# Optimization experiments

Measured on AMD Instinct MI355X. Metric: run time of the kernel, lower is better.

Reference implementation:

```python
import jax, jax.numpy as jnp
import numpy as np

# Static configuration (matches init_kwargs)
L = 3264          # seq_length
K = 12            # ktc=4 -> K=12
LOCC = 4          # ktc=4 -> Locc=4
S, B, A = 8, 64, 4  # streams (user/port pairs), batch, rx antennas
DELAY_MIN, DELAY_MAX = -10, 10


def _phasor(m):
    # m: integer shifts [S, B] -> exp(1j*2*pi*m*n/L) as [S, B, L]
    n = jnp.arange(L, dtype=jnp.int32)
    ang = (2.0 * np.pi / L) * ((m[..., None] * n) % L).astype(jnp.float32)
    return jax.lax.complex(jnp.cos(ang), jnp.sin(ang))


def _linear_interp(h_avg):
    # np.interp with uniform source grid orig[i] = (LOCC-1)/2 + i*LOCC, clamped at ends.
    # h_avg: [S, B, A, R] complex, R = L // LOCC -> [S, B, A, L]
    R = L // LOCC
    new = jnp.arange(L, dtype=jnp.float32)
    t = jnp.clip((new - (LOCC - 1) / 2.0) / LOCC, 0.0, float(R - 1))
    i0 = jnp.floor(t).astype(jnp.int32)
    i1 = jnp.minimum(i0 + 1, R - 1)
    frac = (t - i0).astype(jnp.float32)
    return h_avg[..., i0] * (1.0 - frac) + h_avg[..., i1] * frac


def reference(ls_real, ls_imag, cyclic_shifts, noise_powers):
    ls = jax.lax.complex(ls_real, ls_imag)                     # [S,B,A,L]
    ideal_peak = ((K - cyclic_shifts) % K) * (L // K)          # [S]

    # Stage 1: IFFT + timing-offset search (torch.no_grad in original)
    h_time = jnp.fft.ifft(ls, axis=-1)
    power = jax.lax.stop_gradient(jnp.sum(jnp.abs(h_time) ** 2, axis=2))  # [S,B,L]
    offs = jnp.arange(DELAY_MIN, DELAY_MAX + 1, dtype=jnp.int32)          # [21]
    cand_idx = (ideal_peak[:, None] + offs[None, :]) % L                   # [S,21]
    cand_idx = jnp.broadcast_to(cand_idx[:, None, :], (S, B, offs.shape[0]))
    cand_pow = jnp.take_along_axis(power, cand_idx, axis=-1)               # [S,B,21]
    t_off = offs[jnp.argmax(cand_pow, axis=-1)]                            # [S,B]
    m = t_off + ideal_peak[:, None]                                        # [S,B]
    ph_m = _phasor(m)        # [S,B,L]
    ph_T = _phasor(t_off)    # [S,B,L]

    # Stage 2: phasor shift, OCC demux, interpolation (inside no_grad in original)
    h_shift = ls * ph_m[:, :, None, :]
    h_avg = h_shift.reshape(S, B, A, L // LOCC, LOCC).mean(-1)             # [S,B,A,L/4]
    h_interp = jax.lax.stop_gradient(_linear_interp(h_avg))                # [S,B,A,L]

    # Stage 3: global residual against stream (0,0)'s LS estimate
    total_recon = jnp.sum(h_interp * jnp.conj(ph_m)[:, :, None, :], axis=0)  # [B,A,L]
    residual = ls[0] - total_recon                                           # [B,A,L]

    # Stage 4: apply residual, MMSE (identity: mmse_module=None), timing recovery
    h_wr = h_interp + residual[None, :, :, None, :].squeeze(3) if False else h_interp + residual[None] * ph_m[:, :, None, :]
    final = h_wr * jnp.conj(ph_T)[:, :, None, :]                             # [S,B,A,L]
    return jnp.stack([final.real, final.imag]).astype(jnp.float32)          # [2,S,B,A,L]


def setup_inputs() -> dict:
    key = jax.random.key(0)
    k1, k2, k3, k4 = jax.random.split(key, 4)
    return {
        "ls_real": jax.random.normal(k1, (S, B, A, L), dtype=jnp.float32),
        "ls_imag": jax.random.normal(k2, (S, B, A, L), dtype=jnp.float32),
        "cyclic_shifts": jax.random.randint(k3, (S,), 0, K, dtype=jnp.int32),
        "noise_powers": jax.random.uniform(k4, (B,), dtype=jnp.float32),
    }
```

## Files before the change

kernel.cpp:

```cpp
#include <hip/hip_runtime.h>

namespace {

constexpr int L = 3264;
constexpr int K = 12;
constexpr int S = 8;
constexpr int B = 64;
constexpr int A = 4;
constexpr int R = 816;
constexpr int NOFF = 21;
constexpr int PEAK_STEP = L / K;
constexpr float TWO_PI = 6.28318530717958647692f;
constexpr float CINV = TWO_PI / (float)L;
constexpr int NCHUNK = (L + 255) / 256;

__device__ __forceinline__ float rfl(float x) {
    return __uint_as_float(__builtin_amdgcn_readfirstlane(__float_as_uint(x)));
}

__global__ __launch_bounds__(256)
void k_table(float2* __restrict__ tw)
{
    const int j = blockIdx.x * 256 + threadIdx.x;
    if (j < L) {
        float sv, cv;
        __sincosf(CINV * (float)j, &sv, &cv);
        tw[j] = make_float2(cv, sv);
    }
}

__global__ __launch_bounds__(512)
void k_stage1(const float* __restrict__ lsr, const float* __restrict__ lsi,
              const int* __restrict__ cs, const float2* __restrict__ tw,
              int* __restrict__ toff_out, int* __restrict__ m_out,
              float2* __restrict__ havg)
{
    __shared__ float2 red[8][NOFF];
    __shared__ int m_sh;

    const int sb = blockIdx.x;
    const int s = sb >> 6;
    const int tid = threadIdx.x;
    const int lane = tid & 63;
    const int w = tid >> 6;
    const int a = w >> 1;
    const int h = w & 1;

    const int csv = cs[s];
    const int ideal = ((K - csv) % K) * PEAK_STEP;
    int idx0 = (ideal - 10) % L; if (idx0 < 0) idx0 += L;

    const int k0 = h * 64 + lane;

    const int jb = (k0 * idx0) % L;
    float br, bi; __sincosf(CINV * (float)jb, &bi, &br);
    float lr, li; __sincosf(CINV * (float)k0, &li, &lr);
    float pwr[NOFF], pwi[NOFF];
    pwr[0] = br; pwi[0] = bi;
    #pragma unroll
    for (int d = 1; d < NOFF; ++d) {
        pwr[d] = pwr[d-1] * lr - pwi[d-1] * li;
        pwi[d] = pwr[d-1] * li + pwi[d-1] * lr;
    }

    const int js = (128 * idx0) % L;
    float s0r, s0i; __sincosf(CINV * (float)js, &s0i, &s0r);
    float e8r, e8i; __sincosf(CINV * 128.0f, &e8i, &e8r);
    float str_[NOFF], sti_[NOFF];
    {
        float cr = s0r, ci = s0i;
        #pragma unroll
        for (int d = 0; d < NOFF; ++d) {
            str_[d] = rfl(cr); sti_[d] = rfl(ci);
            const float nr = cr * e8r - ci * e8i;
            ci = cr * e8i + ci * e8r;
            cr = nr;
        }
    }

    const size_t rowbase = ((size_t)sb * A + a) * L;
    const float* __restrict__ pr = lsr + rowbase;
    const float* __restrict__ pi_ = lsi + rowbase;

    float ar[NOFF], ai[NOFF];
    #pragma unroll
    for (int d = 0; d < NOFF; ++d) { ar[d] = 0.f; ai[d] = 0.f; }

    for (int it = 0; it < 25; ++it) {
        const float xr = pr[k0 + (it << 7)];
        const float xi = pi_[k0 + (it << 7)];
        #pragma unroll
        for (int d = 0; d < NOFF; ++d) {
            ar[d] += xr * pwr[d] - xi * pwi[d];
            ai[d] += xr * pwi[d] + xi * pwr[d];
            const float nr = pwr[d] * str_[d] - pwi[d] * sti_[d];
            pwi[d] = pwr[d] * sti_[d] + pwi[d] * str_[d];
            pwr[d] = nr;
        }
    }
    if (k0 < 64) {
        const float xr = pr[k0 + 3200];
        const float xi = pi_[k0 + 3200];
        #pragma unroll
        for (int d = 0; d < NOFF; ++d) {
            ar[d] += xr * pwr[d] - xi * pwi[d];
            ai[d] += xr * pwi[d] + xi * pwr[d];
        }
    }

    #pragma unroll
    for (int d = 0; d < NOFF; ++d) {
        float r = ar[d], im = ai[d];
        #pragma unroll
        for (int o = 32; o > 0; o >>= 1) {
            r  += __shfl_xor(r, o);
            im += __shfl_xor(im, o);
        }
        if (lane == 0) red[w][d] = make_float2(r, im);
    }
    __syncthreads();

    if (w == 0) {
        float pw = -1.f;
        if (lane < NOFF) {
            pw = 0.f;
            #pragma unroll
            for (int a2 = 0; a2 < A; ++a2) {
                const float2 u = red[2 * a2][lane];
                const float2 v = red[2 * a2 + 1][lane];
                const float rr = u.x + v.x;
                const float ii = u.y + v.y;
                pw += rr * rr + ii * ii;
            }
        }
        float mx = pw;
        #pragma unroll
        for (int o = 32; o > 0; o >>= 1) mx = fmaxf(mx, __shfl_xor(mx, o));
        const unsigned long long msk = __ballot(pw == mx);
        const int argd = __ffsll(msk) - 1;
        if (lane == 0) {
            const int toff = argd - 10;
            toff_out[sb] = toff;
            m_out[sb]    = toff + ideal;
            m_sh         = toff + ideal;
        }
    }
    __syncthreads();

    int mp = m_sh % L; if (mp < 0) mp += L;
    const float2 emp = tw[mp];

    for (int aa = 0; aa < A; ++aa) {
        const float4* __restrict__ qr4 = (const float4*)(lsr + ((size_t)sb * A + aa) * L);
        const float4* __restrict__ qi4 = (const float4*)(lsi + ((size_t)sb * A + aa) * L);
        float2* __restrict__ dst = havg + ((size_t)sb * A + aa) * R;
        for (int i = tid; i < R; i += 512) {
            const int j = (mp * (4 * i)) % L;
            const float2 w0 = tw[j];
            const float4 xr = qr4[i];
            const float4 xi = qi4[i];
            float wr = w0.x, wi = w0.y;
            float are, aim, nr;
            are  = xr.x * wr - xi.x * wi;  aim  = xr.x * wi + xi.x * wr;
            nr = wr * emp.x - wi * emp.y;  wi = wr * emp.y + wi * emp.x;  wr = nr;
            are += xr.y * wr - xi.y * wi;  aim += xr.y * wi + xi.y * wr;
            nr = wr * emp.x - wi * emp.y;  wi = wr * emp.y + wi * emp.x;  wr = nr;
            are += xr.z * wr - xi.z * wi;  aim += xr.z * wi + xi.z * wr;
            nr = wr * emp.x - wi * emp.y;  wi = wr * emp.y + wi * emp.x;  wr = nr;
            are += xr.w * wr - xi.w * wi;  aim += xr.w * wi + xi.w * wr;
            dst[i] = make_float2(are * 0.25f, aim * 0.25f);
        }
    }
}

__global__ __launch_bounds__(256)
void k_final(const float* __restrict__ lsr, const float* __restrict__ lsi,
             const int* __restrict__ toff_arr, const int* __restrict__ m_arr,
             const float2* __restrict__ havg, const float2* __restrict__ tw,
             float* __restrict__ out)
{
    const int bid = blockIdx.x;
    const int chunk = bid % NCHUNK;
    const int ba = bid / NCHUNK;
    const int b = ba >> 2;
    const int a = ba & 3;
    const int l = chunk * 256 + (int)threadIdx.x;
    if (l >= L) return;

    float t = ((float)l - 1.5f) * 0.25f;
    t = fminf(fmaxf(t, 0.0f), (float)(R - 1));
    const int i0 = (int)t;
    const int i1 = min(i0 + 1, R - 1);
    const float frac = t - (float)i0;

    float hire[S], hiim[S], pmre[S], pmim[S];
    float rre = 0.f, rim = 0.f;

    #pragma unroll
    for (int s = 0; s < S; ++s) {
        const int sb = s * B + b;
        int mp = m_arr[sb] % L; if (mp < 0) mp += L;
        const float2 wm = tw[(mp * l) % L];
        const float2 h0 = havg[((size_t)sb * A + a) * R + i0];
        const float2 h1 = havg[((size_t)sb * A + a) * R + i1];
        const float hr = h0.x * (1.f - frac) + h1.x * frac;
        const float hi = h0.y * (1.f - frac) + h1.y * frac;
        hire[s] = hr; hiim[s] = hi; pmre[s] = wm.x; pmim[s] = wm.y;
        rre += hr * wm.x + hi * wm.y;
        rim += hi * wm.x - hr * wm.y;
    }

    const size_t off0 = ((size_t)(b * A + a)) * L + l;
    const float resre = lsr[off0] - rre;
    const float resim = lsi[off0] - rim;

    #pragma unroll
    for (int s = 0; s < S; ++s) {
        const float wre = hire[s] + resre * pmre[s] - resim * pmim[s];
        const float wim = hiim[s] + resre * pmim[s] + resim * pmre[s];
        int jt = (toff_arr[s * B + b] * l) % L; if (jt < 0) jt += L;
        const float2 wt = tw[jt];
        const float fre = wre * wt.x + wim * wt.y;
        const float fim = wim * wt.x - wre * wt.y;
        const size_t o = (((size_t)(s * B + b)) * A + a) * L + l;
        __builtin_nontemporal_store(fre, &out[o]);
        __builtin_nontemporal_store(fim, &out[(size_t)S * B * A * L + o]);
    }
}

}

extern "C" void kernel_launch(void* const* d_in, const int* in_sizes, int n_in,
                              void* d_out, int out_size, void* d_ws, size_t ws_size,
                              hipStream_t stream) {
    (void)in_sizes; (void)n_in; (void)out_size; (void)ws_size;
    const float* lsr = (const float*)d_in[0];
    const float* lsi = (const float*)d_in[1];
    const int*   cs  = (const int*)d_in[2];

    int* toff = (int*)d_ws;
    int* marr = toff + 512;
    float2* tw = (float2*)((char*)d_ws + 4096);
    float2* havg = (float2*)((char*)d_ws + 36864);

    k_table<<<NCHUNK, 256, 0, stream>>>(tw);
    k_stage1<<<S * B, 512, 0, stream>>>(lsr, lsi, cs, tw, toff, marr, havg);
    k_final<<<B * A * NCHUNK, 256, 0, stream>>>(lsr, lsi, toff, marr, havg, tw,
                                                (float*)d_out);
}
```

Baseline: 180.8 us.

## Split stage1 into per-antenna DFT, argmax and havg kernels; cache twiddles in LDS

The fused stage1 kernel, one block per stream-batch pair, is split into three kernels. A per-antenna DFT kernel writes candidate powers to a workspace buffer, a small argmax kernel picks the timing offset, and a per-antenna averaging kernel builds havg. This gives four times as many blocks and more parallelism for the DFT and demux work, at the cost of two extra launches and a global round trip for the powers. The final kernel also copies the twiddle table into shared memory so its scattered gathers avoid global loads, at the cost of a per-block preload and sync.

```diff
diff --git a/kernel.cpp b/kernel.cpp
--- a/kernel.cpp
+++ b/kernel.cpp
@@ -29,78 +29,69 @@
     }
 }
 
-__global__ __launch_bounds__(512)
-void k_stage1(const float* __restrict__ lsr, const float* __restrict__ lsi,
-              const int* __restrict__ cs, const float2* __restrict__ tw,
-              int* __restrict__ toff_out, int* __restrict__ m_out,
-              float2* __restrict__ havg)
-{
-    __shared__ float2 red[8][NOFF];
-    __shared__ int m_sh;
-
-    const int sb = blockIdx.x;
+__global__ __launch_bounds__(256)
+void k_dft(const float* __restrict__ lsr, const float* __restrict__ lsi,
+           const int* __restrict__ cs, float* __restrict__ pow_out)
+{
+    __shared__ float2 red[4][NOFF];
+
+    const int blk = blockIdx.x;
+    const int sb = blk >> 2;
+    const int a = blk & 3;
     const int s = sb >> 6;
     const int tid = threadIdx.x;
     const int lane = tid & 63;
     const int w = tid >> 6;
-    const int a = w >> 1;
-    const int h = w & 1;
-
-    const int csv = cs[s];
-    const int ideal = ((K - csv) % K) * PEAK_STEP;
+
+    const int ideal = ((K - cs[s]) % K) * PEAK_STEP;
     int idx0 = (ideal - 10) % L; if (idx0 < 0) idx0 += L;
 
-    const int k0 = h * 64 + lane;
-
-    const int jb = (k0 * idx0) % L;
+    const int jb = (tid * idx0) % L;
     float br, bi; __sincosf(CINV * (float)jb, &bi, &br);
-    float lr, li; __sincosf(CINV * (float)k0, &li, &lr);
-    float pwr[NOFF], pwi[NOFF];
+    float lr, li; __sincosf(CINV * (float)tid, &li, &lr);
+    float pwr[NOFF], pwi[NOFF], ar[NOFF], ai[NOFF];
     pwr[0] = br; pwi[0] = bi;
     #pragma unroll
     for (int d = 1; d < NOFF; ++d) {
         pwr[d] = pwr[d-1] * lr - pwi[d-1] * li;
         pwi[d] = pwr[d-1] * li + pwi[d-1] * lr;
     }
-
-    const int js = (128 * idx0) % L;
+    #pragma unroll
+    for (int d = 0; d < NOFF; ++d) { ar[d] = 0.f; ai[d] = 0.f; }
+
+    const int js = (256 * idx0) % L;
     float s0r, s0i; __sincosf(CINV * (float)js, &s0i, &s0r);
-    float e8r, e8i; __sincosf(CINV * 128.0f, &e8i, &e8r);
+    float c8r, c8i; __sincosf(CINV * 256.0f, &c8i, &c8r);
     float str_[NOFF], sti_[NOFF];
     {
         float cr = s0r, ci = s0i;
         #pragma unroll
         for (int d = 0; d < NOFF; ++d) {
             str_[d] = rfl(cr); sti_[d] = rfl(ci);
-            const float nr = cr * e8r - ci * e8i;
-            ci = cr * e8i + ci * e8r;
-            cr = nr;
-        }
-    }
-
-    const size_t rowbase = ((size_t)sb * A + a) * L;
-    const float* __restrict__ pr = lsr + rowbase;
-    const float* __restrict__ pi_ = lsi + rowbase;
-
-    float ar[NOFF], ai[NOFF];
-    #pragma unroll
-    for (int d = 0; d < NOFF; ++d) { ar[d] = 0.f; ai[d] = 0.f; }
-
-    for (int it = 0; it < 25; ++it) {
-        const float xr = pr[k0 + (it << 7)];
-        const float xi = pi_[k0 + (it << 7)];
+            const float nr2 = cr * c8r - ci * c8i;
+            ci = cr * c8i + ci * c8r;
+            cr = nr2;
+        }
+    }
+
+    const float* __restrict__ pr  = lsr + (size_t)blk * L;
+    const float* __restrict__ pi_ = lsi + (size_t)blk * L;
+
+    for (int it = 0; it < 12; ++it) {
+        const float xr = pr[tid + (it << 8)];
+        const float xi = pi_[tid + (it << 8)];
         #pragma unroll
         for (int d = 0; d < NOFF; ++d) {
             ar[d] += xr * pwr[d] - xi * pwi[d];
             ai[d] += xr * pwi[d] + xi * pwr[d];
-            const float nr = pwr[d] * str_[d] - pwi[d] * sti_[d];
+            const float nr2 = pwr[d] * str_[d] - pwi[d] * sti_[d];
             pwi[d] = pwr[d] * sti_[d] + pwi[d] * str_[d];
-            pwr[d] = nr;
-        }
-    }
-    if (k0 < 64) {
-        const float xr = pr[k0 + 3200];
-        const float xi = pi_[k0 + 3200];
+            pwr[d] = nr2;
+        }
+    }
+    if (tid < 192) {
+        const float xr = pr[tid + 3072];
+        const float xi = pi_[tid + 3072];
         #pragma unroll
         for (int d = 0; d < NOFF; ++d) {
             ar[d] += xr * pwr[d] - xi * pwi[d];
@@ -120,56 +111,71 @@
     }
     __syncthreads();
 
-    if (w == 0) {
-        float pw = -1.f;
-        if (lane < NOFF) {
-            pw = 0.f;
-            #pragma unroll
-            for (int a2 = 0; a2 < A; ++a2) {
-                const float2 u = red[2 * a2][lane];
-                const float2 v = red[2 * a2 + 1][lane];
-                const float rr = u.x + v.x;
-                const float ii = u.y + v.y;
-                pw += rr * rr + ii * ii;
-            }
-        }
-        float mx = pw;
-        #pragma unroll
-        for (int o = 32; o > 0; o >>= 1) mx = fmaxf(mx, __shfl_xor(mx, o));
-        const unsigned long long msk = __ballot(pw == mx);
-        const int argd = __ffsll(msk) - 1;
-        if (lane == 0) {
-            const int toff = argd - 10;
-            toff_out[sb] = toff;
-            m_out[sb]    = toff + ideal;
-            m_sh         = toff + ideal;
-        }
-    }
-    __syncthreads();
-
-    int mp = m_sh % L; if (mp < 0) mp += L;
+    if (w == 0 && lane < NOFF) {
+        float rr = 0.f, ii = 0.f;
+        #pragma unroll
+        for (int q = 0; q < 4; ++q) { rr += red[q][lane].x; ii += red[q][lane].y; }
+        pow_out[sb * (NOFF * A) + lane * A + a] = rr * rr + ii * ii;
+    }
+}
+
+__global__ __launch_bounds__(64)
+void k_argmax(const float* __restrict__ pow_in, const int* __restrict__ cs,
+              int* __restrict__ toff_out, int* __restrict__ m_out)
+{
+    const int sb = blockIdx.x;
+    const int lane = threadIdx.x;
+    const int s = sb >> 6;
+    const int ideal = ((K - cs[s]) % K) * PEAK_STEP;
+
+    float pw = -1.f;
+    if (lane < NOFF) {
+        const float4 p4 = *(const float4*)(pow_in + sb * (NOFF * A) + lane * A);
+        pw = p4.x + p4.y + p4.z + p4.w;
+    }
+    float mx = pw;
+    #pragma unroll
+    for (int o = 32; o > 0; o >>= 1) mx = fmaxf(mx, __shfl_xor(mx, o));
+    const unsigned long long msk = __ballot(pw == mx);
+    const int argd = __ffsll(msk) - 1;
+    if (lane == 0) {
+        const int toff = argd - 10;
+        toff_out[sb] = toff;
+        m_out[sb]    = toff + ideal;
+    }
+}
+
+__global__ __launch_bounds__(256)
+void k_havg(const float* __restrict__ lsr, const float* __restrict__ lsi,
+            const int* __restrict__ m_arr, const float2* __restrict__ tw,
+            float2* __restrict__ havg)
+{
+    const int blk = blockIdx.x;
+    const int sb = blk >> 2;
+    const int tid = threadIdx.x;
+
+    int mp = m_arr[sb] % L; if (mp < 0) mp += L;
     const float2 emp = tw[mp];
 
-    for (int aa = 0; aa < A; ++aa) {
-        const float4* __restrict__ qr4 = (const float4*)(lsr + ((size_t)sb * A + aa) * L);
-        const float4* __restrict__ qi4 = (const float4*)(lsi + ((size_t)sb * A + aa) * L);
-        float2* __restrict__ dst = havg + ((size_t)sb * A + aa) * R;
-        for (int i = tid; i < R; i += 512) {
-            const int j = (mp * (4 * i)) % L;
-            const float2 w0 = tw[j];
-            const float4 xr = qr4[i];
-            const float4 xi = qi4[i];
-            float wr = w0.x, wi = w0.y;
-            float are, aim, nr;
-            are  = xr.x * wr - xi.x * wi;  aim  = xr.x * wi + xi.x * wr;
-            nr = wr * emp.x - wi * emp.y;  wi = wr * emp.y + wi * emp.x;  wr = nr;
-            are += xr.y * wr - xi.y * wi;  aim += xr.y * wi + xi.y * wr;
-            nr = wr * emp.x - wi * emp.y;  wi = wr * emp.y + wi * emp.x;  wr = nr;
-            are += xr.z * wr - xi.z * wi;  aim += xr.z * wi + xi.z * wr;
-            nr = wr * emp.x - wi * emp.y;  wi = wr * emp.y + wi * emp.x;  wr = nr;
-            are += xr.w * wr - xi.w * wi;  aim += xr.w * wi + xi.w * wr;
-            dst[i] = make_float2(are * 0.25f, aim * 0.25f);
-        }
+    const float4* __restrict__ qr4 = (const float4*)(lsr + (size_t)blk * L);
+    const float4* __restrict__ qi4 = (const float4*)(lsi + (size_t)blk * L);
+    float2* __restrict__ dst = havg + (size_t)blk * R;
+
+    for (int i = tid; i < R; i += 256) {
+        const int j = (mp * (4 * i)) % L;
+        const float2 w0 = tw[j];
+        const float4 xr = qr4[i];
+        const float4 xi = qi4[i];
+        float wr = w0.x, wi = w0.y;
+        float are, aim, nr;
+        are  = xr.x * wr - xi.x * wi;  aim  = xr.x * wi + xi.x * wr;
+        nr = wr * emp.x - wi * emp.y;  wi = wr * emp.y + wi * emp.x;  wr = nr;
+        are += xr.y * wr - xi.y * wi;  aim += xr.y * wi + xi.y * wr;
+        nr = wr * emp.x - wi * emp.y;  wi = wr * emp.y + wi * emp.x;  wr = nr;
+        are += xr.z * wr - xi.z * wi;  aim += xr.z * wi + xi.z * wr;
+        nr = wr * emp.x - wi * emp.y;  wi = wr * emp.y + wi * emp.x;  wr = nr;
+        are += xr.w * wr - xi.w * wi;  aim += xr.w * wi + xi.w * wr;
+        dst[i] = make_float2(are * 0.25f, aim * 0.25f);
     }
 }
 
@@ -179,6 +185,10 @@
              const float2* __restrict__ havg, const float2* __restrict__ tw,
              float* __restrict__ out)
 {
+    __shared__ float2 twl[L];
+    for (int j = threadIdx.x; j < L; j += 256) twl[j] = tw[j];
+    __syncthreads();
+
     const int bid = blockIdx.x;
     const int chunk = bid % NCHUNK;
     const int ba = bid / NCHUNK;
@@ -200,7 +210,7 @@
     for (int s = 0; s < S; ++s) {
         const int sb = s * B + b;
         int mp = m_arr[sb] % L; if (mp < 0) mp += L;
-        const float2 wm = tw[(mp * l) % L];
+        const float2 wm = twl[(mp * l) % L];
         const float2 h0 = havg[((size_t)sb * A + a) * R + i0];
         const float2 h1 = havg[((size_t)sb * A + a) * R + i1];
         const float hr = h0.x * (1.f - frac) + h1.x * frac;
@@ -219,7 +229,7 @@
         const float wre = hire[s] + resre * pmre[s] - resim * pmim[s];
         const float wim = hiim[s] + resre * pmim[s] + resim * pmre[s];
         int jt = (toff_arr[s * B + b] * l) % L; if (jt < 0) jt += L;
-        const float2 wt = tw[jt];
+        const float2 wt = twl[jt];
         const float fre = wre * wt.x + wim * wt.y;
         const float fim = wim * wt.x - wre * wt.y;
         const size_t o = (((size_t)(s * B + b)) * A + a) * L + l;
@@ -240,11 +250,14 @@
 
     int* toff = (int*)d_ws;
     int* marr = toff + 512;
-    float2* tw = (float2*)((char*)d_ws + 4096);
-    float2* havg = (float2*)((char*)d_ws + 36864);
-
-    k_table<<<NCHUNK, 256, 0, stream>>>(tw);
-    k_stage1<<<S * B, 512, 0, stream>>>(lsr, lsi, cs, tw, toff, marr, havg);
-    k_final<<<B * A * NCHUNK, 256, 0, stream>>>(lsr, lsi, toff, marr, havg, tw,
-                                                (float*)d_out);
-}
+    float2* tw   = (float2*)((char*)d_ws + 4096);
+    float*  powb = (float*)((char*)d_ws + 30720);
+    float2* havg = (float2*)((char*)d_ws + 204800);
+
+    k_table <<<NCHUNK, 256, 0, stream>>>(tw);
+    k_dft   <<<S * B * A, 256, 0, stream>>>(lsr, lsi, cs, powb);
+    k_argmax<<<S * B, 64, 0, stream>>>(powb, cs, toff, marr);
+    k_havg  <<<S * B * A, 256, 0, stream>>>(lsr, lsi, marr, tw, havg);
+    k_final <<<B * A * NCHUNK, 256, 0, stream>>>(lsr, lsi, toff, marr, havg, tw,
+                                                 (float*)d_out);
+}
```

New measurement: 168.6 us. -6.8%, faster.
